# Kernel tuning notes

Measured on AMD Instinct MI355X. Metric: run time of the kernel, lower is better.

Reference implementation:

```python
import jax, jax.numpy as jnp
import numpy as np


def setup_inputs() -> dict:
    key = jax.random.key(0)
    k1, k2, k3, k4 = jax.random.split(key, 4)
    B, N, M, D = 8, 2048, 2048, 256
    x = jax.random.normal(k1, (B, N, D), dtype=jnp.float32)
    Fi = jax.random.normal(k2, (B, M, D), dtype=jnp.float32)
    # nn.Linear(dim, dim) params (W applied as x @ W.T + b); scale like torch default
    bound = 1.0 / np.sqrt(D)
    W = jax.random.uniform(k3, (D, D), dtype=jnp.float32, minval=-bound, maxval=bound)
    b = jax.random.uniform(k4, (D,), dtype=jnp.float32, minval=-bound, maxval=bound)
    return {"x": x, "Fi": Fi, "W": W, "b": b}


def reference(x, Fi, W, b):
    # x: [B, N, D], Fi: [B, M, D]
    q = jnp.einsum("bnd,ed->bne", x, W) + b          # linear projection
    scores = jnp.einsum("bnd,bmd->bnm", q, Fi)        # QK^T (no scaling in original)
    attn = jax.nn.softmax(scores, axis=-1)            # softmax over keys
    out = jnp.einsum("bnm,bmd->bnd", attn, Fi)        # attention @ V (V = Fi)
    return out
```

## Files before the change

### kernel.cpp

```cpp
#include <hip/hip_runtime.h>
#include <hip/hip_bf16.h>

typedef _Float16 half8 __attribute__((ext_vector_type(8)));
typedef float floatx4 __attribute__((ext_vector_type(4)));

#define MFMA16H(a, b, c) __builtin_amdgcn_mfma_f32_16x16x32_f16((a), (b), (c), 0, 0, 0)

static constexpr int Bb = 8, Nn = 2048, Mm = 2048, Dd = 256;

__device__ inline void async16(const void* g, void* l)
{
    __builtin_amdgcn_global_load_lds((const __attribute__((address_space(1))) unsigned int*)g,
                                     (__attribute__((address_space(3))) unsigned int*)l,
                                     16, 0, 0);
}

__device__ inline half8 cvt8h(const float* __restrict__ p)
{
    float4 f0 = *reinterpret_cast<const float4*>(p);
    float4 f1 = *reinterpret_cast<const float4*>(p + 4);
    half8 r;
    r[0] = (_Float16)f0.x; r[1] = (_Float16)f0.y; r[2] = (_Float16)f0.z; r[3] = (_Float16)f0.w;
    r[4] = (_Float16)f1.x; r[5] = (_Float16)f1.y; r[6] = (_Float16)f1.z; r[7] = (_Float16)f1.w;
    return r;
}

__device__ inline void cvt8h_split(const float* __restrict__ p, half8& h, half8& l)
{
    float4 f0 = *reinterpret_cast<const float4*>(p);
    float4 f1 = *reinterpret_cast<const float4*>(p + 4);
    float f[8] = {f0.x, f0.y, f0.z, f0.w, f1.x, f1.y, f1.z, f1.w};
#pragma unroll
    for (int i = 0; i < 8; ++i) {
        _Float16 hh = (_Float16)f[i];
        h[i] = hh;
        l[i] = (_Float16)(f[i] - (float)hh);
    }
}

__global__ __launch_bounds__(256, 4)
void prep_kernel(const float* __restrict__ Fi, const float* __restrict__ W,
                 _Float16* __restrict__ FiH, _Float16* __restrict__ FiT,
                 _Float16* __restrict__ Wh, _Float16* __restrict__ Wl)
{
    const int bid = blockIdx.x;
    const int t = threadIdx.x;

    if (bid >= 1024) {
        const size_t base = (size_t)(bid - 1024) * 2048 + t * 8;
        half8 h, l;
        cvt8h_split(W + base, h, l);
        *(half8*)(Wh + base) = h;
        *(half8*)(Wl + base) = l;
        return;
    }

    __shared__ __align__(16) unsigned short tile[64][72];
    const int b  = bid >> 7;
    const int mt = (bid >> 2) & 31;
    const int dt = bid & 3;
    {
        const int i = t >> 2, jc = (t & 3) * 16;
        const float* src = Fi + ((size_t)b * Mm + mt * 64 + i) * Dd + dt * 64 + jc;
        union { half8 v; uint4 u; } p0, p1;
        p0.v = cvt8h(src);
        p1.v = cvt8h(src + 8);
        *(uint4*)&tile[i][jc]     = p0.u;
        *(uint4*)&tile[i][jc + 8] = p1.u;
        unsigned short* dh = reinterpret_cast<unsigned short*>(FiH)
            + ((size_t)b * Mm + mt * 64 + i) * Dd + dt * 64 + jc;
        *(uint4*)dh       = p0.u;
        *(uint4*)(dh + 8) = p1.u;
    }
    __syncthreads();
    {
        const int d = t >> 2, mc = (t & 3) * 16;
        unsigned short* dst = reinterpret_cast<unsigned short*>(FiT)
            + ((size_t)b * Dd + dt * 64 + d) * Mm + mt * 64 + mc;
        union { uint4 v[2]; unsigned short s[16]; } u;
#pragma unroll
        for (int s = 0; s < 16; ++s) u.s[s] = tile[mc + s][d];
        *(uint4*)dst       = u.v[0];
        *(uint4*)(dst + 8) = u.v[1];
    }
}

__global__ __launch_bounds__(128, 4)
void qproj_kernel(const float* __restrict__ x, const _Float16* __restrict__ Wh,
                  const _Float16* __restrict__ Wl, const float* __restrict__ bias,
                  _Float16* __restrict__ q)
{
    const int lane = threadIdx.x & 63;
    const int w = threadIdx.x >> 6;
    const int lo = lane & 15, hi = lane >> 4;
    const long r0 = (long)blockIdx.x * 16;

    floatx4 acc[8];
#pragma unroll
    for (int j = 0; j < 8; ++j) acc[j] = (floatx4)0.0f;

#pragma unroll
    for (int kk = 0; kk < 8; ++kk) {
        half8 ah, al;
        cvt8h_split(x + (size_t)(r0 + lo) * Dd + kk * 32 + hi * 8, ah, al);
#pragma unroll
        for (int j = 0; j < 8; ++j) {
            const int e = (w * 8 + j) * 16 + lo;
            const size_t wb = (size_t)e * Dd + kk * 32 + hi * 8;
            half8 bh = *reinterpret_cast<const half8*>(Wh + wb);
            half8 bl = *reinterpret_cast<const half8*>(Wl + wb);
            acc[j] = MFMA16H(ah, bh, acc[j]);
            acc[j] = MFMA16H(ah, bl, acc[j]);
            acc[j] = MFMA16H(al, bh, acc[j]);
        }
    }
#pragma unroll
    for (int j = 0; j < 8; ++j) {
        const int e = (w * 8 + j) * 16 + lo;
        const float bv = bias[e];
#pragma unroll
        for (int r = 0; r < 4; ++r)
            q[(size_t)(r0 + hi * 4 + r) * Dd + e] = (_Float16)(acc[j][r] + bv);
    }
}

__global__ __launch_bounds__(256, 2)
void flash_kernel(const _Float16* __restrict__ q, const _Float16* __restrict__ FiH,
                  const _Float16* __restrict__ FiT, _Float16* __restrict__ o_part,
                  float* __restrict__ m_part, float* __restrict__ l_part)
{
    __shared__ __align__(16) _Float16 sFiA[32 * 256];
    __shared__ __align__(16) _Float16 sFiB[32 * 256];
    __shared__ __align__(16) _Float16 sFiTA[256 * 32];
    __shared__ __align__(16) _Float16 sFiTB[256 * 32];
    __shared__ __align__(16) _Float16 sP[4][32 * 36];

    const int bid = blockIdx.x;
    const int b  = bid & 7;
    const int u  = bid >> 3;
    const int nt = u & 15;
    const int kh = u >> 4;
    const int tid = threadIdx.x;
    const int lane = tid & 63, w = tid >> 6;
    const int lo = lane & 15, hi = lane >> 4;
    const int nbase = nt * 128 + w * 32;

    const _Float16* fH = FiH + (size_t)b * Mm * Dd;
    const _Float16* fT = FiT + (size_t)b * Dd * Mm;

    half8 qf[2][8];
    const _Float16* qb = q + ((size_t)b * Nn + nbase + lo) * Dd + hi * 8;
#pragma unroll
    for (int rt = 0; rt < 2; ++rt)
#pragma unroll
        for (int kk = 0; kk < 8; ++kk)
            qf[rt][kk] = *reinterpret_cast<const half8*>(qb + rt * 16 * Dd + kk * 32);

    half8 ones;
#pragma unroll
    for (int i = 0; i < 8; ++i) ones[i] = (_Float16)1.0f;

    floatx4 o[2][16];
    floatx4 ol[2];
#pragma unroll
    for (int rt = 0; rt < 2; ++rt) {
#pragma unroll
        for (int t = 0; t < 16; ++t) o[rt][t] = (floatx4)0.0f;
        ol[rt] = (floatx4)0.0f;
    }
    float m_i[2][4];
#pragma unroll
    for (int rt = 0; rt < 2; ++rt)
#pragma unroll
        for (int r = 0; r < 4; ++r) m_i[rt][r] = -INFINITY;

    auto stage = [&](int it, _Float16* dFi, _Float16* dFiT) {
        const int key0 = kh * 512 + it * 32;
#pragma unroll
        for (int j = 0; j < 4; ++j) {
            const int rbase = (w * 4 + j) * 2;
            const int r = rbase + (lane >> 5);
            const int gc = (lane & 31) ^ (r & 7);
            async16(fH + (size_t)(key0 + r) * Dd + gc * 8, dFi + rbase * 256);
        }
#pragma unroll
        for (int j = 0; j < 4; ++j) {
            const int rbase = (w + j * 4) * 16;
            const int r = rbase + (lane >> 2);
            const int gc = (lane & 3) ^ (r & 3);
            async16(fT + (size_t)r * Mm + key0 + gc * 8, dFiT + rbase * 32);
        }
    };

    auto compute = [&](const _Float16* SFI, const _Float16* SFIT) {
        floatx4 s[2][2];
#pragma unroll
        for (int rt = 0; rt < 2; ++rt)
#pragma unroll
            for (int st = 0; st < 2; ++st) s[rt][st] = (floatx4)0.0f;
#pragma unroll
        for (int st = 0; st < 2; ++st) {
            const int row = st * 16 + lo;
#pragma unroll
            for (int kk = 0; kk < 8; ++kk) {
                half8 bv = *reinterpret_cast<const half8*>(
                    SFI + row * 256 + (((kk * 4 + hi) ^ (lo & 7)) * 8));
                s[0][st] = MFMA16H(qf[0][kk], bv, s[0][st]);
                s[1][st] = MFMA16H(qf[1][kk], bv, s[1][st]);
            }
        }

        float mn[2][4];
        bool chg = false;
#pragma unroll
        for (int rt = 0; rt < 2; ++rt)
#pragma unroll
            for (int r = 0; r < 4; ++r) {
                float mc = fmaxf(s[rt][0][r], s[rt][1][r]);
                mc = fmaxf(mc, __shfl_xor(mc, 1));
                mc = fmaxf(mc, __shfl_xor(mc, 2));
                mc = fmaxf(mc, __shfl_xor(mc, 4));
                mc = fmaxf(mc, __shfl_xor(mc, 8));
                mn[rt][r] = fmaxf(m_i[rt][r], mc);
                chg = chg || (mn[rt][r] > m_i[rt][r]);
            }
        if (__any(chg)) {
#pragma unroll
            for (int rt = 0; rt < 2; ++rt) {
                float al4[4];
#pragma unroll
                for (int r = 0; r < 4; ++r) {
                    al4[r] = __expf(m_i[rt][r] - mn[rt][r]);
                    m_i[rt][r] = mn[rt][r];
                }
#pragma unroll
                for (int t = 0; t < 16; ++t) {
                    floatx4 ot = o[rt][t];
#pragma unroll
                    for (int r = 0; r < 4; ++r) ot[r] *= al4[r];
                    o[rt][t] = ot;
                }
#pragma unroll
                for (int r = 0; r < 4; ++r) ol[rt][r] *= al4[r];
            }
        }
#pragma unroll
        for (int rt = 0; rt < 2; ++rt)
#pragma unroll
            for (int r = 0; r < 4; ++r) {
                _Float16 p0 = (_Float16)__expf(s[rt][0][r] - m_i[rt][r]);
                _Float16 p1 = (_Float16)__expf(s[rt][1][r] - m_i[rt][r]);
                sP[w][(rt * 16 + hi * 4 + r) * 36 + lo]      = p0;
                sP[w][(rt * 16 + hi * 4 + r) * 36 + 16 + lo] = p1;
            }

        half8 pa0 = *reinterpret_cast<const half8*>(&sP[w][lo * 36 + hi * 8]);
        half8 pa1 = *reinterpret_cast<const half8*>(&sP[w][(16 + lo) * 36 + hi * 8]);
#pragma unroll
        for (int t = 0; t < 16; ++t) {
            half8 bv = *reinterpret_cast<const half8*>(
                SFIT + (t * 16 + lo) * 32 + ((hi ^ (lo & 3)) * 8));
            o[0][t] = MFMA16H(pa0, bv, o[0][t]);
            o[1][t] = MFMA16H(pa1, bv, o[1][t]);
        }
        ol[0] = MFMA16H(pa0, ones, ol[0]);
        ol[1] = MFMA16H(pa1, ones, ol[1]);
    };

    stage(0, sFiA, sFiTA);
    for (int it = 0; it < 16; it += 2) {
        __syncthreads();
        stage(it + 1, sFiB, sFiTB);
        compute(sFiA, sFiTA);
        __syncthreads();
        if (it + 2 < 16) stage(it + 2, sFiA, sFiTA);
        compute(sFiB, sFiTB);
    }

#pragma unroll
    for (int rt = 0; rt < 2; ++rt)
#pragma unroll
        for (int r = 0; r < 4; ++r) {
            const long gq = (long)b * Nn + nbase + rt * 16 + hi * 4 + r;
            const size_t obase = ((size_t)kh * (Bb * Nn) + gq) * Dd;
#pragma unroll
            for (int t = 0; t < 16; ++t)
                o_part[obase + t * 16 + lo] = (_Float16)o[rt][t][r];
            if (lo == 0) {
                m_part[(size_t)kh * (Bb * Nn) + gq] = m_i[rt][r];
                l_part[(size_t)kh * (Bb * Nn) + gq] = ol[rt][r];
            }
        }
}

__global__ __launch_bounds__(256, 8)
void merge_kernel(const _Float16* __restrict__ o_part, const float* __restrict__ m_part,
                  const float* __restrict__ l_part, float* __restrict__ out)
{
    const int row = blockIdx.x;
    const int col = threadIdx.x;
    float m[4], l[4];
#pragma unroll
    for (int k = 0; k < 4; ++k) {
        m[k] = m_part[(size_t)k * (Bb * Nn) + row];
        l[k] = l_part[(size_t)k * (Bb * Nn) + row];
    }
    float M = fmaxf(fmaxf(m[0], m[1]), fmaxf(m[2], m[3]));
    float denom = 0.f, acc = 0.f;
#pragma unroll
    for (int k = 0; k < 4; ++k) {
        const float wk = __expf(m[k] - M);
        denom += wk * l[k];
        acc += wk * (float)o_part[((size_t)k * (Bb * Nn) + row) * Dd + col];
    }
    out[(size_t)row * Dd + col] = acc / denom;
}

extern "C" void kernel_launch(void* const* d_in, const int* in_sizes, int n_in,
                              void* d_out, int out_size, void* d_ws, size_t ws_size,
                              hipStream_t stream)
{
    const float* x    = (const float*)d_in[0];
    const float* Fi   = (const float*)d_in[1];
    const float* W    = (const float*)d_in[2];
    const float* bias = (const float*)d_in[3];
    float* out = (float*)d_out;

    _Float16* q_ws = (_Float16*)d_ws;
    _Float16* FiH  = q_ws + (size_t)Bb * Nn * Dd;
    _Float16* FiT  = FiH + (size_t)Bb * Mm * Dd;
    _Float16* Wh   = FiT + (size_t)Bb * Dd * Mm;
    _Float16* Wl   = Wh + (size_t)Dd * Dd;
    _Float16* o_part = Wl + (size_t)Dd * Dd;
    float* m_part  = (float*)(o_part + (size_t)4 * Bb * Nn * Dd);
    float* l_part  = m_part + (size_t)4 * Bb * Nn;

    hipLaunchKernelGGL(prep_kernel, dim3(1056), dim3(256), 0, stream, Fi, W, FiH, FiT, Wh, Wl);
    hipLaunchKernelGGL(qproj_kernel, dim3(1024), dim3(128), 0, stream, x, Wh, Wl, bias, q_ws);
    hipLaunchKernelGGL(flash_kernel, dim3(512), dim3(256), 0, stream, q_ws, FiH, FiT,
                       o_part, m_part, l_part);
    hipLaunchKernelGGL(merge_kernel, dim3(16384), dim3(256), 0, stream, o_part, m_part, l_part, out);
}
```

Baseline: 231.9 us.

## Stage W tiles in LDS for qproj and pack P stores via key permutation

The q-projection kernel now handles 32 rows per block with 256 threads. It stages the fp16 hi/lo W slices into swizzled LDS tiles through async global-to-LDS loads, so each W fragment is reused across two row tiles instead of being read from global memory for every block. In the flash kernel, FiH rows are loaded in a permuted key order so that each lane's two score columns map to adjacent keys. That lets P be written as packed 32-bit pairs into a 40-element-padded LDS buffer, halving the LDS stores for P. The cost is extra barriers per k-step in qproj and fewer qproj blocks.

```diff
diff --git a/kernel.cpp b/kernel.cpp
--- a/kernel.cpp
+++ b/kernel.cpp
@@ -85,42 +85,65 @@
     }
 }
 
-__global__ __launch_bounds__(128, 4)
+__global__ __launch_bounds__(256, 2)
 void qproj_kernel(const float* __restrict__ x, const _Float16* __restrict__ Wh,
                   const _Float16* __restrict__ Wl, const float* __restrict__ bias,
                   _Float16* __restrict__ q)
 {
-    const int lane = threadIdx.x & 63;
-    const int w = threadIdx.x >> 6;
+    __shared__ __align__(16) _Float16 sWh[256 * 32];
+    __shared__ __align__(16) _Float16 sWl[256 * 32];
+
+    const int tid = threadIdx.x;
+    const int lane = tid & 63, w = tid >> 6;
     const int lo = lane & 15, hi = lane >> 4;
-    const long r0 = (long)blockIdx.x * 16;
-
-    floatx4 acc[8];
-#pragma unroll
-    for (int j = 0; j < 8; ++j) acc[j] = (floatx4)0.0f;
-
-#pragma unroll
-    for (int kk = 0; kk < 8; ++kk) {
-        half8 ah, al;
-        cvt8h_split(x + (size_t)(r0 + lo) * Dd + kk * 32 + hi * 8, ah, al);
-#pragma unroll
-        for (int j = 0; j < 8; ++j) {
-            const int e = (w * 8 + j) * 16 + lo;
-            const size_t wb = (size_t)e * Dd + kk * 32 + hi * 8;
-            half8 bh = *reinterpret_cast<const half8*>(Wh + wb);
-            half8 bl = *reinterpret_cast<const half8*>(Wl + wb);
-            acc[j] = MFMA16H(ah, bh, acc[j]);
-            acc[j] = MFMA16H(ah, bl, acc[j]);
-            acc[j] = MFMA16H(al, bh, acc[j]);
-        }
-    }
-#pragma unroll
-    for (int j = 0; j < 8; ++j) {
-        const int e = (w * 8 + j) * 16 + lo;
+    const long r0 = (long)blockIdx.x * 32;
+
+    floatx4 acc[2][4];
+#pragma unroll
+    for (int rt = 0; rt < 2; ++rt)
+#pragma unroll
+        for (int j = 0; j < 4; ++j) acc[rt][j] = (floatx4)0.0f;
+
+    const int se = lane >> 2, sc = lane & 3;
+
+    for (int k0 = 0; k0 < 256; k0 += 32) {
+        __syncthreads();
+#pragma unroll
+        for (int j = 0; j < 4; ++j) {
+            const int e0 = (w * 4 + j) * 16;
+            const int e = e0 + se;
+            const int gc = sc ^ (e & 3);
+            async16(Wh + (size_t)e * Dd + k0 + gc * 8, sWh + e0 * 32);
+            async16(Wl + (size_t)e * Dd + k0 + gc * 8, sWl + e0 * 32);
+        }
+        __syncthreads();
+
+        half8 ah[2], al[2];
+#pragma unroll
+        for (int rt = 0; rt < 2; ++rt)
+            cvt8h_split(x + (size_t)(r0 + rt * 16 + lo) * Dd + k0 + hi * 8, ah[rt], al[rt]);
+#pragma unroll
+        for (int jj = 0; jj < 4; ++jj) {
+            const int e = (w * 4 + jj) * 16 + lo;
+            half8 bh = *reinterpret_cast<const half8*>(&sWh[(e & 255) * 32 + ((hi ^ (e & 3)) * 8)]);
+            half8 bl = *reinterpret_cast<const half8*>(&sWl[(e & 255) * 32 + ((hi ^ (e & 3)) * 8)]);
+#pragma unroll
+            for (int rt = 0; rt < 2; ++rt) {
+                acc[rt][jj] = MFMA16H(ah[rt], bh, acc[rt][jj]);
+                acc[rt][jj] = MFMA16H(ah[rt], bl, acc[rt][jj]);
+                acc[rt][jj] = MFMA16H(al[rt], bh, acc[rt][jj]);
+            }
+        }
+    }
+#pragma unroll
+    for (int jj = 0; jj < 4; ++jj) {
+        const int e = (w * 4 + jj) * 16 + lo;
         const float bv = bias[e];
 #pragma unroll
-        for (int r = 0; r < 4; ++r)
-            q[(size_t)(r0 + hi * 4 + r) * Dd + e] = (_Float16)(acc[j][r] + bv);
+        for (int rt = 0; rt < 2; ++rt)
+#pragma unroll
+            for (int r = 0; r < 4; ++r)
+                q[(size_t)(r0 + rt * 16 + hi * 4 + r) * Dd + e] = (_Float16)(acc[rt][jj][r] + bv);
     }
 }
 
@@ -133,7 +156,7 @@
     __shared__ __align__(16) _Float16 sFiB[32 * 256];
     __shared__ __align__(16) _Float16 sFiTA[256 * 32];
     __shared__ __align__(16) _Float16 sFiTB[256 * 32];
-    __shared__ __align__(16) _Float16 sP[4][32 * 36];
+    __shared__ __align__(16) _Float16 sP[4][32 * 40];
 
     const int bid = blockIdx.x;
     const int b  = bid & 7;
@@ -180,8 +203,9 @@
         for (int j = 0; j < 4; ++j) {
             const int rbase = (w * 4 + j) * 2;
             const int r = rbase + (lane >> 5);
+            const int kp = 2 * (r & 15) + (r >> 4);
             const int gc = (lane & 31) ^ (r & 7);
-            async16(fH + (size_t)(key0 + r) * Dd + gc * 8, dFi + rbase * 256);
+            async16(fH + (size_t)(key0 + kp) * Dd + gc * 8, dFi + rbase * 256);
         }
 #pragma unroll
         for (int j = 0; j < 4; ++j) {
@@ -248,14 +272,15 @@
         for (int rt = 0; rt < 2; ++rt)
 #pragma unroll
             for (int r = 0; r < 4; ++r) {
-                _Float16 p0 = (_Float16)__expf(s[rt][0][r] - m_i[rt][r]);
-                _Float16 p1 = (_Float16)__expf(s[rt][1][r] - m_i[rt][r]);
-                sP[w][(rt * 16 + hi * 4 + r) * 36 + lo]      = p0;
-                sP[w][(rt * 16 + hi * 4 + r) * 36 + 16 + lo] = p1;
-            }
-
-        half8 pa0 = *reinterpret_cast<const half8*>(&sP[w][lo * 36 + hi * 8]);
-        half8 pa1 = *reinterpret_cast<const half8*>(&sP[w][(16 + lo) * 36 + hi * 8]);
+                union { _Float16 h[2]; unsigned u; } pk;
+                pk.h[0] = (_Float16)__expf(s[rt][0][r] - m_i[rt][r]);
+                pk.h[1] = (_Float16)__expf(s[rt][1][r] - m_i[rt][r]);
+                *reinterpret_cast<unsigned*>(
+                    &sP[w][(rt * 16 + hi * 4 + r) * 40 + 2 * lo]) = pk.u;
+            }
+
+        half8 pa0 = *reinterpret_cast<const half8*>(&sP[w][lo * 40 + hi * 8]);
+        half8 pa1 = *reinterpret_cast<const half8*>(&sP[w][(16 + lo) * 40 + hi * 8]);
 #pragma unroll
         for (int t = 0; t < 16; ++t) {
             half8 bv = *reinterpret_cast<const half8*>(
@@ -336,7 +361,7 @@
     float* l_part  = m_part + (size_t)4 * Bb * Nn;
 
     hipLaunchKernelGGL(prep_kernel, dim3(1056), dim3(256), 0, stream, Fi, W, FiH, FiT, Wh, Wl);
-    hipLaunchKernelGGL(qproj_kernel, dim3(1024), dim3(128), 0, stream, x, Wh, Wl, bias, q_ws);
+    hipLaunchKernelGGL(qproj_kernel, dim3(512), dim3(256), 0, stream, x, Wh, Wl, bias, q_ws);
     hipLaunchKernelGGL(flash_kernel, dim3(512), dim3(256), 0, stream, q_ws, FiH, FiT,
                        o_part, m_part, l_part);
     hipLaunchKernelGGL(merge_kernel, dim3(16384), dim3(256), 0, stream, o_part, m_part, l_part, out);
```

Result: faster. 216.7 us (-6.6%).
